# Kernel optimization log

Measured on AMD Instinct MI355X. Metric: run time of the kernel, lower is better.

Reference implementation:

```python
import jax, jax.numpy as jnp
import numpy as np

N_NODES = 100000
N_EDGES = 1600000
IN_FEATS, HIDDEN, OUT_MU, OUT_LV = 256, 128, 64, 64


def setup_inputs() -> dict:
    key = jax.random.key(0)
    ks = jax.random.split(key, 8)
    X = jax.random.normal(ks[0], (N_NODES, IN_FEATS), dtype=jnp.float32)
    edge_index = jax.random.randint(ks[1], (2, N_EDGES), 0, N_NODES, dtype=jnp.int64)
    def glorot(k, shape):
        lim = np.sqrt(6.0 / (shape[0] + shape[1])).astype(np.float32)
        return jax.random.uniform(k, shape, jnp.float32, -lim, lim)
    W1 = glorot(ks[2], (IN_FEATS, HIDDEN))
    b1 = jnp.zeros((HIDDEN,), jnp.float32)
    Wmu = glorot(ks[3], (HIDDEN, OUT_MU))
    bmu = jnp.zeros((OUT_MU,), jnp.float32)
    Wlv = glorot(ks[4], (HIDDEN, OUT_LV))
    blv = jnp.zeros((OUT_LV,), jnp.float32)
    return {"X": X, "edge_index": edge_index, "W1": W1, "b1": b1,
            "Wmu": Wmu, "bmu": bmu, "Wlv": Wlv, "blv": blv}


def _gcn_norm(edge_index, num_nodes):
    # Add self-loops (PyG GCNConv default) and compute symmetric normalization.
    loop = jnp.arange(num_nodes, dtype=edge_index.dtype)
    row = jnp.concatenate([edge_index[0], loop])  # source
    col = jnp.concatenate([edge_index[1], loop])  # target
    deg = jax.ops.segment_sum(jnp.ones_like(col, dtype=jnp.float32), col,
                              num_segments=num_nodes)
    dinv = jnp.where(deg > 0, jax.lax.rsqrt(deg), 0.0)
    norm = dinv[row] * dinv[col]  # [E+N]
    return row, col, norm


def _gcn_conv(x, W, b, row, col, norm, num_nodes):
    # Linear transform, then normalized sparse neighbor aggregation at targets.
    h = x @ W                                   # [N, F_out]
    msg = h[row] * norm[:, None]                # gather + scale, [E+N, F_out]
    out = jax.ops.segment_sum(msg, col, num_segments=num_nodes)
    return out + b


def reference(X, edge_index, W1, b1, Wmu, bmu, Wlv, blv):
    n = X.shape[0]
    row, col, norm = _gcn_norm(edge_index, n)
    H = jax.nn.relu(_gcn_conv(X, W1, b1, row, col, norm, n))
    mu = _gcn_conv(H, Wmu, bmu, row, col, norm, n)
    lv = _gcn_conv(H, Wlv, blv, row, col, norm, n)
    return (mu, lv)
```

## Files before the change

### kernel.cpp

```cpp
#include <hip/hip_runtime.h>
#include <hip/hip_bf16.h>
#include <cstdint>

#define N_FEATS_IN 256
#define HID 128
#define OUTF 64
#define NBMAX 400
#define BCAP 6144
#define XS_STRIDE 264

typedef __bf16 bf16x8 __attribute__((ext_vector_type(8)));
typedef __bf16 bf16x4 __attribute__((ext_vector_type(4)));
typedef __bf16 bf16x2 __attribute__((ext_vector_type(2)));
typedef float f32x4 __attribute__((ext_vector_type(4)));


__global__ __launch_bounds__(256) void bucket_count(const int* __restrict__ ei, int E,
    int CH, int NB, int* __restrict__ gbk, int* __restrict__ bbase) {
  __shared__ int cnt[NBMAX];
  const int t = threadIdx.x, blk = blockIdx.x;
  for (int i = t; i < NB; i += 256) cnt[i] = 0;
  __syncthreads();
  int base = blk * CH, lim = min(base + CH, E);
  for (int i = base + t; i < lim; i += 256) atomicAdd(&cnt[ei[E + i] >> 8], 1);
  __syncthreads();
  for (int i = t; i < NB; i += 256) {
    int b = (i + blk) % NB;
    int v = cnt[b];
    bbase[(size_t)blk * NB + b] = (v > 0) ? atomicAdd(&gbk[b], v) : 0;
  }
}

__global__ __launch_bounds__(512) void bucket_scan(const int* __restrict__ gbk,
    int* __restrict__ gbkoff, int NB, int E) {
  __shared__ int ts[512];
  const int t = threadIdx.x;
  int v = (t < NB) ? gbk[t] : 0;
  ts[t] = v;
  __syncthreads();
  for (int off = 1; off < 512; off <<= 1) {
    int u = (t >= off) ? ts[t - off] : 0;
    __syncthreads();
    ts[t] += u;
    __syncthreads();
  }
  if (t < NB) gbkoff[t] = ts[t] - v;
  if (t == 0) gbkoff[NB] = E;
}

__global__ __launch_bounds__(256) void bucket_scatter(const int* __restrict__ ei, int E,
    int CH, int NB, const int* __restrict__ gbkoff, const int* __restrict__ bbase,
    int2* __restrict__ bucketed) {
  __shared__ int cur[NBMAX];
  const int t = threadIdx.x, blk = blockIdx.x;
  for (int i = t; i < NB; i += 256)
    cur[i] = gbkoff[i] + bbase[(size_t)blk * NB + i];
  __syncthreads();
  int base = blk * CH, lim = min(base + CH, E);
  for (int i = base + t; i < lim; i += 256) {
    int s = ei[i];
    int c = ei[E + i];
    int p = atomicAdd(&cur[c >> 8], 1);
    bucketed[p] = make_int2(s, c);
  }
}

__global__ __launch_bounds__(256) void bucket_csr(const int2* __restrict__ bucketed,
    const int* __restrict__ gbkoff, int NB, int N, int E,
    float* __restrict__ dinv, int* __restrict__ ptr, int* __restrict__ csrc) {
  __shared__ int2 eb[BCAP];
  __shared__ int cnt[256], scn[256], cur[256];
  const int b = blockIdx.x, t = threadIdx.x;
  const int beg = gbkoff[b], end = gbkoff[b + 1];
  const int M = end - beg;
  cnt[t] = 0;
  __syncthreads();
  const bool inlds = (M <= BCAP);
  if (inlds) {
    for (int i = t; i < M; i += 256) {
      int2 r = bucketed[beg + i];
      eb[i] = r;
      atomicAdd(&cnt[r.y & 255], 1);
    }
  } else {
    for (int i = t; i < M; i += 256) atomicAdd(&cnt[bucketed[beg + i].y & 255], 1);
  }
  __syncthreads();
  const int c0 = cnt[t];
  scn[t] = c0;
  __syncthreads();
  for (int off = 1; off < 256; off <<= 1) {
    int u = (t >= off) ? scn[t - off] : 0;
    __syncthreads();
    scn[t] += u;
    __syncthreads();
  }
  const int excl = scn[t] - c0;
  const int node = b * 256 + t;
  if (node < N) {
    ptr[node] = beg + excl;
    dinv[node] = rsqrtf((float)(c0 + 1));
  }
  if (b == NB - 1 && t == 0) ptr[N] = E;
  cur[t] = excl;
  __syncthreads();
  if (inlds) {
    for (int i = t; i < M; i += 256) {
      int2 r = eb[i];
      int slot = atomicAdd(&cur[r.y & 255], 1);
      csrc[beg + slot] = r.x;
    }
  } else {
    for (int i = t; i < M; i += 256) {
      int2 r = bucketed[beg + i];
      int slot = atomicAdd(&cur[r.y & 255], 1);
      csrc[beg + slot] = r.x;
    }
  }
}


__global__ __launch_bounds__(256) void pack_all_kernel(const float* __restrict__ W1,
    const float* __restrict__ Wmu, const float* __restrict__ Wlv,
    __bf16* __restrict__ W1p, __bf16* __restrict__ Wcp) {
  int idx = blockIdx.x * 256 + threadIdx.x;
  if (idx < 32768) {
    int j = idx & 7, l = (idx >> 3) & 63, t = (idx >> 9) & 7, s = idx >> 12;
    int k = s * 32 + (l >> 4) * 8 + j;
    int n = t * 16 + (l & 15);
    W1p[idx] = (__bf16)W1[k * HID + n];
  } else if (idx < 49152) {
    int i2 = idx - 32768;
    int j = i2 & 7, l = (i2 >> 3) & 63, t = (i2 >> 9) & 7, s = i2 >> 12;
    int k = s * 32 + (l >> 4) * 8 + j;
    int g = t * 16 + (l & 15);
    float v = (g < OUTF) ? Wmu[k * OUTF + g] : Wlv[k * OUTF + (g - OUTF)];
    Wcp[i2] = (__bf16)v;
  }
}


__global__ __launch_bounds__(256) void gemm1_mfma(const float* __restrict__ X,
    const __bf16* __restrict__ Wp, const float* __restrict__ dinv,
    __bf16* __restrict__ Yb, int nrows) {
  __shared__ __bf16 xs[128 * XS_STRIDE];
  const int tid = threadIdx.x;
  const int rowbase = blockIdx.x * 128;

#pragma unroll
  for (int i = 0; i < 32; ++i) {
    int idx = i * 256 + tid;
    int row = idx >> 6;
    int cc = idx & 63;
    int gr = min(rowbase + row, nrows - 1);
    float4 v = ((const float4*)(X + (size_t)gr * N_FEATS_IN))[cc];
    bf16x4 b;
    b[0] = (__bf16)v.x; b[1] = (__bf16)v.y; b[2] = (__bf16)v.z; b[3] = (__bf16)v.w;
    *(bf16x4*)(xs + row * XS_STRIDE + cc * 4) = b;
  }
  __syncthreads();

  const int lane = tid & 63;
  const int wave = tid >> 6;
  const int lm = lane & 15;
  const int q = lane >> 4;
  const bf16x8* wp = (const bf16x8*)Wp;

  f32x4 acc[2][8];
#pragma unroll
  for (int m = 0; m < 2; ++m)
#pragma unroll
    for (int t = 0; t < 8; ++t) acc[m][t] = (f32x4)0.f;

#pragma unroll
  for (int s = 0; s < 8; ++s) {
    bf16x8 a0 = *(const bf16x8*)(xs + (wave * 32 + lm) * XS_STRIDE + s * 32 + q * 8);
    bf16x8 a1 = *(const bf16x8*)(xs + (wave * 32 + 16 + lm) * XS_STRIDE + s * 32 + q * 8);
#pragma unroll
    for (int t = 0; t < 8; ++t) {
      bf16x8 b = wp[(s * 8 + t) * 64 + lane];
      acc[0][t] = __builtin_amdgcn_mfma_f32_16x16x32_bf16(a0, b, acc[0][t], 0, 0, 0);
      acc[1][t] = __builtin_amdgcn_mfma_f32_16x16x32_bf16(a1, b, acc[1][t], 0, 0, 0);
    }
  }

  float dd[2][4];
#pragma unroll
  for (int m = 0; m < 2; ++m)
#pragma unroll
    for (int r2 = 0; r2 < 4; ++r2) {
      int row = rowbase + wave * 32 + m * 16 + q * 4 + r2;
      dd[m][r2] = (row < nrows) ? dinv[row] : 0.f;
    }

#pragma unroll
  for (int m = 0; m < 2; ++m) {
    int rb = rowbase + wave * 32 + m * 16 + q * 4;
#pragma unroll
    for (int t = 0; t < 8; ++t) {
#pragma unroll
      for (int r2 = 0; r2 < 4; ++r2) {
        int row = rb + r2;
        if (row < nrows)
          Yb[(size_t)row * HID + t * 16 + lm] = (__bf16)(acc[m][t][r2] * dd[m][r2]);
      }
    }
  }
}


__global__ __launch_bounds__(256) void agg_kernel(const __bf16* __restrict__ Fin,
    const int* __restrict__ ptr, const int* __restrict__ csrc,
    const float* __restrict__ dinv, const float* __restrict__ bias,
    __bf16* __restrict__ Fout, int do_relu, int N) {
  const int tid = threadIdx.x;
  const int lane = tid & 63;
  const int half = lane >> 5;
  const int l = lane & 31;
  const int c = blockIdx.x * 8 + (tid >> 6) * 2 + half;
  if (c >= N) return;

  const float d = dinv[c];
  bf16x4 sv = ((const bf16x4*)(Fin + (size_t)c * HID))[l];
  float a0 = (float)sv[0], a1 = (float)sv[1], a2 = (float)sv[2], a3 = (float)sv[3];

  const int beg = ptr[c], end = ptr[c + 1];
  int e = beg;
  for (; e + 8 <= end; e += 8) {
    int r[8];
#pragma unroll
    for (int i = 0; i < 8; ++i) r[i] = csrc[e + i];
    bf16x4 v[8];
#pragma unroll
    for (int i = 0; i < 8; ++i) v[i] = ((const bf16x4*)(Fin + (size_t)r[i] * HID))[l];
#pragma unroll
    for (int i = 0; i < 8; ++i) {
      a0 += (float)v[i][0];
      a1 += (float)v[i][1];
      a2 += (float)v[i][2];
      a3 += (float)v[i][3];
    }
  }
  for (; e < end; ++e) {
    int r = csrc[e];
    bf16x4 v = ((const bf16x4*)(Fin + (size_t)r * HID))[l];
    a0 += (float)v[0];
    a1 += (float)v[1];
    a2 += (float)v[2];
    a3 += (float)v[3];
  }

  if (do_relu) {
    float4 bv = ((const float4*)bias)[l];
    a0 = fmaxf(fmaf(d, a0, bv.x), 0.f) * d;
    a1 = fmaxf(fmaf(d, a1, bv.y), 0.f) * d;
    a2 = fmaxf(fmaf(d, a2, bv.z), 0.f) * d;
    a3 = fmaxf(fmaf(d, a3, bv.w), 0.f) * d;
  } else {
    a0 *= d; a1 *= d; a2 *= d; a3 *= d;
  }
  bf16x4 o;
  o[0] = (__bf16)a0; o[1] = (__bf16)a1; o[2] = (__bf16)a2; o[3] = (__bf16)a3;
  ((bf16x4*)(Fout + (size_t)c * HID))[l] = o;
}


__global__ __launch_bounds__(256) void gemm2_mfma(const __bf16* __restrict__ Gb,
    const __bf16* __restrict__ Wp, const float* __restrict__ bmu,
    const float* __restrict__ blv, float* __restrict__ out, int nrows, int ntiles) {
  __shared__ __bf16 bs[16384];
  const int tid = threadIdx.x;
  {
    const float4* s4 = (const float4*)Wp;
    float4* d4 = (float4*)bs;
#pragma unroll
    for (int i = 0; i < 8; ++i) d4[tid + 256 * i] = s4[tid + 256 * i];
  }
  __syncthreads();
  const int lane = tid & 63;
  const int wave = tid >> 6;
  const int lm = lane & 15;
  const int q = lane >> 4;
  const bf16x8* bsv = (const bf16x8*)bs;

  float bv[8];
  size_t obase[8];
#pragma unroll
  for (int t = 0; t < 8; ++t) {
    int col = t * 16 + lm;
    bv[t] = (col < OUTF) ? bmu[col] : blv[col - OUTF];
    obase[t] = (col < OUTF) ? (size_t)col : ((size_t)nrows * OUTF + (col - OUTF));
  }

  for (int tile = blockIdx.x; tile < ntiles; tile += gridDim.x) {
    const int row0 = tile * 64 + wave * 16;
    const int r = min(row0 + lm, nrows - 1);
    const bf16x8* gp = (const bf16x8*)(Gb + (size_t)r * HID);

    bf16x8 xa[4];
#pragma unroll
    for (int s = 0; s < 4; ++s) xa[s] = gp[s * 4 + q];

    f32x4 acc[8];
#pragma unroll
    for (int t = 0; t < 8; ++t) acc[t] = (f32x4)0.f;

#pragma unroll
    for (int s = 0; s < 4; ++s) {
#pragma unroll
      for (int t = 0; t < 8; ++t)
        acc[t] = __builtin_amdgcn_mfma_f32_16x16x32_bf16(xa[s], bsv[(s * 8 + t) * 64 + lane],
                                                         acc[t], 0, 0, 0);
    }
#pragma unroll
    for (int t = 0; t < 8; ++t) {
#pragma unroll
      for (int r2 = 0; r2 < 4; ++r2) {
        int row = row0 + q * 4 + r2;
        if (row < nrows) out[obase[t] + (size_t)row * OUTF] = acc[t][r2] + bv[t];
      }
    }
  }
}


extern "C" void kernel_launch(void* const* d_in, const int* in_sizes, int n_in,
                              void* d_out, int out_size, void* d_ws, size_t ws_size,
                              hipStream_t stream) {
  const float* X   = (const float*)d_in[0];
  const int*   ei  = (const int*)d_in[1];
  const float* W1  = (const float*)d_in[2];
  const float* b1  = (const float*)d_in[3];
  const float* Wmu = (const float*)d_in[4];
  const float* bmu = (const float*)d_in[5];
  const float* Wlv = (const float*)d_in[6];
  const float* blv = (const float*)d_in[7];
  float* out = (float*)d_out;

  const int N = in_sizes[0] / N_FEATS_IN;
  const int E = in_sizes[1] / 2;

  char* ws = (char*)d_ws;
  size_t off = 0;
  auto alloc = [&](size_t bytes) -> void* {
    void* p = ws + off;
    off += (bytes + 255) & ~(size_t)255;
    return p;
  };
  __bf16* Yb   = (__bf16*)alloc((size_t)N * HID * 2);
  __bf16* Hb   = (__bf16*)alloc((size_t)N * HID * 2);
  float* dinv  = (float*)alloc((size_t)N * 4);
  int*   ptr   = (int*)alloc((size_t)(N + 1) * 4);
  int2*  bucketed = (int2*)alloc((size_t)E * 8);
  int*   csrc  = (int*)alloc((size_t)E * 4);
  int*   gbk   = (int*)alloc((size_t)NBMAX * 4);
  int*   gbkoff = (int*)alloc((size_t)(NBMAX + 1) * 4);
  int*   bbase = (int*)alloc((size_t)256 * NBMAX * 4);
  __bf16* W1p  = (__bf16*)alloc(32768 * 2);
  __bf16* Wcp  = (__bf16*)alloc(16384 * 2);
  (void)ws_size; (void)n_in; (void)out_size;

  const int NB = (N + 255) >> 8;
  const int P = 256;
  const int CH = (E + P - 1) / P;

  hipMemsetAsync(gbk, 0, (size_t)NB * 4, stream);
  bucket_count<<<P, 256, 0, stream>>>(ei, E, CH, NB, gbk, bbase);
  bucket_scan<<<1, 512, 0, stream>>>(gbk, gbkoff, NB, E);
  bucket_scatter<<<P, 256, 0, stream>>>(ei, E, CH, NB, gbkoff, bbase, bucketed);
  bucket_csr<<<NB, 256, 0, stream>>>(bucketed, gbkoff, NB, N, E, dinv, ptr, csrc);
  pack_all_kernel<<<192, 256, 0, stream>>>(W1, Wmu, Wlv, W1p, Wcp);

  int g1 = (N + 127) / 128;
  gemm1_mfma<<<g1, 256, 0, stream>>>(X, W1p, dinv, Yb, N);
  int ga = (N + 7) / 8;
  agg_kernel<<<ga, 256, 0, stream>>>(Yb, ptr, csrc, dinv, b1, Hb, 1, N);
  agg_kernel<<<ga, 256, 0, stream>>>(Hb, ptr, csrc, dinv, b1, Yb, 0, N);
  int ntiles2 = (N + 63) / 64;
  int g2 = ntiles2 < 768 ? ntiles2 : 768;
  gemm2_mfma<<<g2, 256, 0, stream>>>(Yb, Wcp, bmu, blv, out, N, ntiles2);
}
```

Measured before the change: 409.7 us.

## Slice feature matrices into 16-column planes and load GEMM1 inputs directly

```diff
diff --git a/kernel.cpp b/kernel.cpp
--- a/kernel.cpp
+++ b/kernel.cpp
@@ -7,12 +7,12 @@
 #define OUTF 64
 #define NBMAX 400
 #define BCAP 6144
-#define XS_STRIDE 264
 
 typedef __bf16 bf16x8 __attribute__((ext_vector_type(8)));
 typedef __bf16 bf16x4 __attribute__((ext_vector_type(4)));
 typedef __bf16 bf16x2 __attribute__((ext_vector_type(2)));
 typedef float f32x4 __attribute__((ext_vector_type(4)));
+
 
 
 __global__ __launch_bounds__(256) void bucket_count(const int* __restrict__ ei, int E,
@@ -143,27 +143,18 @@
 __global__ __launch_bounds__(256) void gemm1_mfma(const float* __restrict__ X,
     const __bf16* __restrict__ Wp, const float* __restrict__ dinv,
     __bf16* __restrict__ Yb, int nrows) {
-  __shared__ __bf16 xs[128 * XS_STRIDE];
   const int tid = threadIdx.x;
-  const int rowbase = blockIdx.x * 128;
-
-#pragma unroll
-  for (int i = 0; i < 32; ++i) {
-    int idx = i * 256 + tid;
-    int row = idx >> 6;
-    int cc = idx & 63;
-    int gr = min(rowbase + row, nrows - 1);
-    float4 v = ((const float4*)(X + (size_t)gr * N_FEATS_IN))[cc];
-    bf16x4 b;
-    b[0] = (__bf16)v.x; b[1] = (__bf16)v.y; b[2] = (__bf16)v.z; b[3] = (__bf16)v.w;
-    *(bf16x4*)(xs + row * XS_STRIDE + cc * 4) = b;
-  }
-  __syncthreads();
-
   const int lane = tid & 63;
   const int wave = tid >> 6;
   const int lm = lane & 15;
   const int q = lane >> 4;
+  const int rowbase = blockIdx.x * 128 + wave * 32;
+
+  const int r0 = min(rowbase + lm, nrows - 1);
+  const int r1 = min(rowbase + 16 + lm, nrows - 1);
+  const float* x0 = X + (size_t)r0 * N_FEATS_IN + q * 8;
+  const float* x1 = X + (size_t)r1 * N_FEATS_IN + q * 8;
+
   const bf16x8* wp = (const bf16x8*)Wp;
 
   f32x4 acc[2][8];
@@ -174,8 +165,15 @@
 
 #pragma unroll
   for (int s = 0; s < 8; ++s) {
-    bf16x8 a0 = *(const bf16x8*)(xs + (wave * 32 + lm) * XS_STRIDE + s * 32 + q * 8);
-    bf16x8 a1 = *(const bf16x8*)(xs + (wave * 32 + 16 + lm) * XS_STRIDE + s * 32 + q * 8);
+    float4 l0 = *(const float4*)(x0 + s * 32);
+    float4 h0 = *(const float4*)(x0 + s * 32 + 4);
+    float4 l1 = *(const float4*)(x1 + s * 32);
+    float4 h1 = *(const float4*)(x1 + s * 32 + 4);
+    bf16x8 a0, a1;
+    a0[0] = (__bf16)l0.x; a0[1] = (__bf16)l0.y; a0[2] = (__bf16)l0.z; a0[3] = (__bf16)l0.w;
+    a0[4] = (__bf16)h0.x; a0[5] = (__bf16)h0.y; a0[6] = (__bf16)h0.z; a0[7] = (__bf16)h0.w;
+    a1[0] = (__bf16)l1.x; a1[1] = (__bf16)l1.y; a1[2] = (__bf16)l1.z; a1[3] = (__bf16)l1.w;
+    a1[4] = (__bf16)h1.x; a1[5] = (__bf16)h1.y; a1[6] = (__bf16)h1.z; a1[7] = (__bf16)h1.w;
 #pragma unroll
     for (int t = 0; t < 8; ++t) {
       bf16x8 b = wp[(s * 8 + t) * 64 + lane];
@@ -189,20 +187,21 @@
   for (int m = 0; m < 2; ++m)
 #pragma unroll
     for (int r2 = 0; r2 < 4; ++r2) {
-      int row = rowbase + wave * 32 + m * 16 + q * 4 + r2;
+      int row = rowbase + m * 16 + q * 4 + r2;
       dd[m][r2] = (row < nrows) ? dinv[row] : 0.f;
     }
 
 #pragma unroll
   for (int m = 0; m < 2; ++m) {
-    int rb = rowbase + wave * 32 + m * 16 + q * 4;
+    int rb = rowbase + m * 16 + q * 4;
 #pragma unroll
     for (int t = 0; t < 8; ++t) {
+      __bf16* yslice = Yb + (size_t)t * nrows * 16;
 #pragma unroll
       for (int r2 = 0; r2 < 4; ++r2) {
         int row = rb + r2;
         if (row < nrows)
-          Yb[(size_t)row * HID + t * 16 + lm] = (__bf16)(acc[m][t][r2] * dd[m][r2]);
+          yslice[(size_t)row * 16 + lm] = (__bf16)(acc[m][t][r2] * dd[m][r2]);
       }
     }
   }
@@ -214,14 +213,16 @@
     const float* __restrict__ dinv, const float* __restrict__ bias,
     __bf16* __restrict__ Fout, int do_relu, int N) {
   const int tid = threadIdx.x;
-  const int lane = tid & 63;
-  const int half = lane >> 5;
-  const int l = lane & 31;
-  const int c = blockIdx.x * 8 + (tid >> 6) * 2 + half;
+  const int s = blockIdx.x & 7;
+  const int tb = blockIdx.x >> 3;
+  const int g = tid >> 2;
+  const int fl = tid & 3;
+  const int c = tb * 64 + g;
   if (c >= N) return;
 
+  const __bf16* F = Fin + (size_t)s * N * 16;
   const float d = dinv[c];
-  bf16x4 sv = ((const bf16x4*)(Fin + (size_t)c * HID))[l];
+  bf16x4 sv = ((const bf16x4*)(F + (size_t)c * 16))[fl];
   float a0 = (float)sv[0], a1 = (float)sv[1], a2 = (float)sv[2], a3 = (float)sv[3];
 
   const int beg = ptr[c], end = ptr[c + 1];
@@ -232,7 +233,7 @@
     for (int i = 0; i < 8; ++i) r[i] = csrc[e + i];
     bf16x4 v[8];
 #pragma unroll
-    for (int i = 0; i < 8; ++i) v[i] = ((const bf16x4*)(Fin + (size_t)r[i] * HID))[l];
+    for (int i = 0; i < 8; ++i) v[i] = ((const bf16x4*)(F + (size_t)r[i] * 16))[fl];
 #pragma unroll
     for (int i = 0; i < 8; ++i) {
       a0 += (float)v[i][0];
@@ -243,7 +244,7 @@
   }
   for (; e < end; ++e) {
     int r = csrc[e];
-    bf16x4 v = ((const bf16x4*)(Fin + (size_t)r * HID))[l];
+    bf16x4 v = ((const bf16x4*)(F + (size_t)r * 16))[fl];
     a0 += (float)v[0];
     a1 += (float)v[1];
     a2 += (float)v[2];
@@ -251,7 +252,7 @@
   }
 
   if (do_relu) {
-    float4 bv = ((const float4*)bias)[l];
+    float4 bv = ((const float4*)bias)[s * 4 + fl];
     a0 = fmaxf(fmaf(d, a0, bv.x), 0.f) * d;
     a1 = fmaxf(fmaf(d, a1, bv.y), 0.f) * d;
     a2 = fmaxf(fmaf(d, a2, bv.z), 0.f) * d;
@@ -261,7 +262,7 @@
   }
   bf16x4 o;
   o[0] = (__bf16)a0; o[1] = (__bf16)a1; o[2] = (__bf16)a2; o[3] = (__bf16)a3;
-  ((bf16x4*)(Fout + (size_t)c * HID))[l] = o;
+  ((bf16x4*)(Fout + (size_t)s * N * 16 + (size_t)c * 16))[fl] = o;
 }
 
 
@@ -295,21 +296,24 @@
   for (int tile = blockIdx.x; tile < ntiles; tile += gridDim.x) {
     const int row0 = tile * 64 + wave * 16;
     const int r = min(row0 + lm, nrows - 1);
-    const bf16x8* gp = (const bf16x8*)(Gb + (size_t)r * HID);
 
     bf16x8 xa[4];
 #pragma unroll
-    for (int s = 0; s < 4; ++s) xa[s] = gp[s * 4 + q];
+    for (int si = 0; si < 4; ++si) {
+      int chunk = si * 4 + q;
+      xa[si] = *(const bf16x8*)(Gb + (size_t)(chunk >> 1) * nrows * 16 +
+                                (size_t)r * 16 + (chunk & 1) * 8);
+    }
 
     f32x4 acc[8];
 #pragma unroll
     for (int t = 0; t < 8; ++t) acc[t] = (f32x4)0.f;
 
 #pragma unroll
-    for (int s = 0; s < 4; ++s) {
+    for (int si = 0; si < 4; ++si) {
 #pragma unroll
       for (int t = 0; t < 8; ++t)
-        acc[t] = __builtin_amdgcn_mfma_f32_16x16x32_bf16(xa[s], bsv[(s * 8 + t) * 64 + lane],
+        acc[t] = __builtin_amdgcn_mfma_f32_16x16x32_bf16(xa[si], bsv[(si * 8 + t) * 64 + lane],
                                                          acc[t], 0, 0, 0);
     }
 #pragma unroll
@@ -373,7 +377,7 @@
 
   int g1 = (N + 127) / 128;
   gemm1_mfma<<<g1, 256, 0, stream>>>(X, W1p, dinv, Yb, N);
-  int ga = (N + 7) / 8;
+  int ga = ((N + 63) / 64) * 8;
   agg_kernel<<<ga, 256, 0, stream>>>(Yb, ptr, csrc, dinv, b1, Hb, 1, N);
   agg_kernel<<<ga, 256, 0, stream>>>(Hb, ptr, csrc, dinv, b1, Yb, 0, N);
   int ntiles2 = (N + 63) / 64;
```

Result: slower. 452.4 us (+10.4%).
